# Performance work log

Measured on AMD Instinct MI355X. Metric: run time of the kernel, lower is better.

Reference implementation:

```python
import jax, jax.numpy as jnp
import numpy as np

# Constants from GaussianSplattingCompliance.__init__
SCALE_MIN, SCALE_MAX = 0.05, 1.5
RATIO_MIN, RATIO_MAX = 0.5, 3.5
ROT_MIN, ROT_MAX = -np.pi / 2, np.pi / 2
AXIS_OFFSET = 0.05
EMIN = 1e-9
SMOOTH_K = 10.0

N_POINTS = 131072  # number of FE element centers (512x256 mesh, flattened)
N_G = 256          # number of gaussians (args['args']['N_g'])


def setup_inputs() -> dict:
    key = jax.random.key(0)
    k0, k1, k2, k3, k4 = jax.random.split(key, 5)
    coords = jax.random.uniform(k0, (N_POINTS, 2), dtype=jnp.float32)
    W_scale = jax.random.normal(k1, (N_G, 1), dtype=jnp.float32)
    W_shape_var = jax.random.normal(k2, (N_G, 1), dtype=jnp.float32)
    W_rotation = jax.random.normal(k3, (N_G, 1), dtype=jnp.float32)
    W_offsets = jax.random.normal(k4, (N_G, 2), dtype=jnp.float32)
    return {"coords": coords, "W_scale": W_scale, "W_shape_var": W_shape_var,
            "W_rotation": W_rotation, "W_offsets": W_offsets}


def reference(coords, W_scale, W_shape_var, W_rotation, W_offsets):
    # coord bounds are constant buffers in the original module (computed once in __init__)
    c = jax.lax.stop_gradient(coords)
    cmin, cmax = c.min(axis=0), c.max(axis=0)                      # (2,)
    coord_min = cmin - cmax * AXIS_OFFSET
    coord_max = cmax + cmax * AXIS_OFFSET

    B = W_scale.shape[0]
    base_scale = (SCALE_MAX - SCALE_MIN) * jax.nn.sigmoid(W_scale)[:, 0] + SCALE_MIN   # (B,)
    ratio = (RATIO_MAX - RATIO_MIN) * jax.nn.sigmoid(W_shape_var) + RATIO_MIN          # (B,1)
    sigmas = jnp.concatenate([jnp.ones((B, 1), coords.dtype), ratio], axis=1)          # (B,2)
    rotation = ROT_MIN + (ROT_MAX - ROT_MIN) * jax.nn.sigmoid(W_rotation)[:, 0]        # (B,)
    offsets = coord_min + (coord_max - coord_min) * jax.nn.sigmoid(W_offsets)          # (B,2)

    cos_r, sin_r = jnp.cos(rotation), jnp.sin(rotation)
    R = jnp.stack([jnp.stack([cos_r, -sin_r], axis=-1),
                   jnp.stack([sin_r, cos_r], axis=-1)], axis=-2)                       # (B,2,2)
    inv_cov_diag = 1.0 / (sigmas ** 2 + 1e-6)                                          # (B,2)

    # (B, N, 2): centered, scaled coordinates per gaussian
    xy = (coords[None, :, :] - offsets[:, None, :]) / (base_scale[:, None, None] + 1e-8)
    rxy = jnp.einsum('bij,bnj->bni', R, xy)                                            # (B,N,2)
    # diagonal Mahalanobis quadratic form
    z = jnp.sqrt(jnp.einsum('bni,bi,bni->bn', rxy, inv_cov_diag, rxy))                 # (B,N)
    kernel = jax.nn.sigmoid(-10.0 * (z - 1.0))                                         # 1/(1+exp(10(z-1)))
    kernel_sum = kernel.sum(axis=0) + 1e-8                                             # (N,)
    H = (1.0 - EMIN) * jax.nn.sigmoid(-SMOOTH_K * (kernel_sum - 0.5)) + EMIN           # (N,)
    return H
```

## Files before the change

### kernel.cpp

```cpp
#include <hip/hip_runtime.h>
#include <cmath>

#define N_GAUSS 256

__global__ __launch_bounds__(256) void k_partial_minmax(
    const float2* __restrict__ coords, int n, float4* __restrict__ partial) {
  int tid = blockIdx.x * blockDim.x + threadIdx.x;
  int stride = gridDim.x * blockDim.x;
  float mnx = INFINITY, mny = INFINITY, mxx = -INFINITY, mxy = -INFINITY;
  for (int i = tid; i < n; i += stride) {
    float2 c = coords[i];
    mnx = fminf(mnx, c.x);
    mny = fminf(mny, c.y);
    mxx = fmaxf(mxx, c.x);
    mxy = fmaxf(mxy, c.y);
  }
  for (int o = 32; o > 0; o >>= 1) {
    mnx = fminf(mnx, __shfl_down(mnx, o));
    mny = fminf(mny, __shfl_down(mny, o));
    mxx = fmaxf(mxx, __shfl_down(mxx, o));
    mxy = fmaxf(mxy, __shfl_down(mxy, o));
  }
  __shared__ float4 lds[4];
  if ((threadIdx.x & 63) == 0) lds[threadIdx.x >> 6] = make_float4(mnx, mny, mxx, mxy);
  __syncthreads();
  if (threadIdx.x == 0) {
    float4 r = lds[0];
    for (int w = 1; w < 4; ++w) {
      float4 o = lds[w];
      r.x = fminf(r.x, o.x);
      r.y = fminf(r.y, o.y);
      r.z = fmaxf(r.z, o.z);
      r.w = fmaxf(r.w, o.w);
    }
    partial[blockIdx.x] = r;
  }
}

__device__ __forceinline__ float sigmoidf_fast(float w) {
  float t = __builtin_amdgcn_exp2f(-1.4426950408889634f * w);
  return 1.0f / (1.0f + t);
}

__global__ __launch_bounds__(256) void k_fused_main(
    const float2* __restrict__ coords,
    const float4* __restrict__ partial,
    const float* __restrict__ W_scale,
    const float* __restrict__ W_shape_var,
    const float* __restrict__ W_rotation,
    const float* __restrict__ W_offsets,
    float* __restrict__ out, int n) {
  __shared__ float4 sp[2 * N_GAUSS];
  __shared__ float4 lds4[4];
  __shared__ float4 boundsS;

  int t = threadIdx.x;

  float4 r = partial[t];
  for (int o = 32; o > 0; o >>= 1) {
    r.x = fminf(r.x, __shfl_down(r.x, o));
    r.y = fminf(r.y, __shfl_down(r.y, o));
    r.z = fmaxf(r.z, __shfl_down(r.z, o));
    r.w = fmaxf(r.w, __shfl_down(r.w, o));
  }
  if ((t & 63) == 0) lds4[t >> 6] = r;
  __syncthreads();
  if (t == 0) {
    float4 a = lds4[0];
    for (int w = 1; w < 4; ++w) {
      float4 o = lds4[w];
      a.x = fminf(a.x, o.x);
      a.y = fminf(a.y, o.y);
      a.z = fmaxf(a.z, o.z);
      a.w = fmaxf(a.w, o.w);
    }
    boundsS = a;
  }
  __syncthreads();
  float4 bc = boundsS;

  {
    float cmin0 = bc.x - bc.z * 0.05f;
    float cmin1 = bc.y - bc.w * 0.05f;
    float cmax0 = bc.z + bc.z * 0.05f;
    float cmax1 = bc.w + bc.w * 0.05f;

    float sS = sigmoidf_fast(W_scale[t]);
    float base_scale = 1.45f * sS + 0.05f;
    float sV = sigmoidf_fast(W_shape_var[t]);
    float ratio = 3.0f * sV + 0.5f;
    float sR = sigmoidf_fast(W_rotation[t]);
    const float PIf = 3.14159265358979323846f;
    float rot = -0.5f * PIf + PIf * sR;
    float sOx = sigmoidf_fast(W_offsets[2 * t]);
    float sOy = sigmoidf_fast(W_offsets[2 * t + 1]);
    float ox = cmin0 + (cmax0 - cmin0) * sOx;
    float oy = cmin1 + (cmax1 - cmin1) * sOy;

    float cr = cosf(rot), sr = sinf(rot);
    float inv_s = 1.0f / (base_scale + 1e-8f);
    float r0 = rsqrtf(1.0f + 1e-6f);
    float r1 = rsqrtf(fmaf(ratio, ratio, 1e-6f));

    float A = r0 * cr * inv_s;
    float B = -r0 * sr * inv_s;
    float E = -fmaf(A, ox, B * oy);
    float C = r1 * sr * inv_s;
    float D = r1 * cr * inv_s;
    float F = -fmaf(C, ox, D * oy);

    sp[2 * t]     = make_float4(A, B, E, C);
    sp[2 * t + 1] = make_float4(D, F, 0.0f, 0.0f);
  }
  __syncthreads();

  int i = blockIdx.x * blockDim.x + threadIdx.x;
  if (i >= n) return;
  float2 c = coords[i];
  float x = c.x, y = c.y;
  float ks = 1e-8f;
  const float K1 = 14.4269504088896339f;

  for (int b0 = 0; b0 < N_GAUSS; b0 += 8) {
#pragma unroll
    for (int j = 0; j < 8; ++j) {
      int b = b0 + j;
      float4 p0 = sp[2 * b];
      float4 p1 = sp[2 * b + 1];
      float u = fmaf(p0.x, x, fmaf(p0.y, y, p0.z));
      float v = fmaf(p0.w, x, fmaf(p1.x, y, p1.y));
      float z = sqrtf(fmaf(u, u, v * v));
      float tt = __builtin_amdgcn_exp2f(fmaf(K1, z, -K1));
      ks += __builtin_amdgcn_rcpf(1.0f + tt);
    }
    if (__all(ks > 6.0f)) break;
  }

  float t2 = __builtin_amdgcn_exp2f(fmaf(K1, ks, -0.5f * K1));
  float s = __builtin_amdgcn_rcpf(1.0f + t2);
  out[i] = fmaf(1e-9f, 1.0f - s, s);
}

extern "C" void kernel_launch(void* const* d_in, const int* in_sizes, int n_in,
                              void* d_out, int out_size, void* d_ws, size_t ws_size,
                              hipStream_t stream) {
  const float* coords      = (const float*)d_in[0];
  const float* W_scale     = (const float*)d_in[1];
  const float* W_shape_var = (const float*)d_in[2];
  const float* W_rotation  = (const float*)d_in[3];
  const float* W_offsets   = (const float*)d_in[4];
  float* out = (float*)d_out;

  int n = in_sizes[0] / 2;

  float4* partial = (float4*)d_ws;

  k_partial_minmax<<<256, 256, 0, stream>>>((const float2*)coords, n, partial);
  int blocks = (n + 255) / 256;
  k_fused_main<<<blocks, 256, 0, stream>>>((const float2*)coords, partial,
                                           W_scale, W_shape_var, W_rotation,
                                           W_offsets, out, n);
}
```

Baseline: 66.85 us.

## Process two points per thread and vectorize coord loads; shrink minmax grid

```diff
diff --git a/kernel.cpp b/kernel.cpp
--- a/kernel.cpp
+++ b/kernel.cpp
@@ -4,12 +4,21 @@
 #define N_GAUSS 256
 
 __global__ __launch_bounds__(256) void k_partial_minmax(
-    const float2* __restrict__ coords, int n, float4* __restrict__ partial) {
+    const float4* __restrict__ coords4, int m ,
+    const float2* __restrict__ coords, int n,
+    float4* __restrict__ partial) {
   int tid = blockIdx.x * blockDim.x + threadIdx.x;
   int stride = gridDim.x * blockDim.x;
   float mnx = INFINITY, mny = INFINITY, mxx = -INFINITY, mxy = -INFINITY;
-  for (int i = tid; i < n; i += stride) {
-    float2 c = coords[i];
+  for (int i = tid; i < m; i += stride) {
+    float4 c = coords4[i];
+    mnx = fminf(mnx, fminf(c.x, c.z));
+    mny = fminf(mny, fminf(c.y, c.w));
+    mxx = fmaxf(mxx, fmaxf(c.x, c.z));
+    mxy = fmaxf(mxy, fmaxf(c.y, c.w));
+  }
+  if (tid == 0 && (n & 1)) {
+    float2 c = coords[n - 1];
     mnx = fminf(mnx, c.x);
     mny = fminf(mny, c.y);
     mxx = fmaxf(mxx, c.x);
@@ -43,6 +52,7 @@
 }
 
 __global__ __launch_bounds__(256) void k_fused_main(
+    const float4* __restrict__ coords4,
     const float2* __restrict__ coords,
     const float4* __restrict__ partial,
     const float* __restrict__ W_scale,
@@ -56,7 +66,8 @@
 
   int t = threadIdx.x;
 
-  float4 r = partial[t];
+  float4 r = (t < 64) ? partial[t]
+                      : make_float4(INFINITY, INFINITY, -INFINITY, -INFINITY);
   for (int o = 32; o > 0; o >>= 1) {
     r.x = fminf(r.x, __shfl_down(r.x, o));
     r.y = fminf(r.y, __shfl_down(r.y, o));
@@ -114,31 +125,54 @@
   }
   __syncthreads();
 
-  int i = blockIdx.x * blockDim.x + threadIdx.x;
-  if (i >= n) return;
-  float2 c = coords[i];
-  float x = c.x, y = c.y;
-  float ks = 1e-8f;
+  int gid = blockIdx.x * blockDim.x + threadIdx.x;
+  int i0 = 2 * gid;
+  if (i0 >= n) return;
+  bool has2 = (i0 + 1) < n;
+
+  float x0, y0, x1, y1;
+  if (has2) {
+    float4 c = coords4[gid];
+    x0 = c.x; y0 = c.y; x1 = c.z; y1 = c.w;
+  } else {
+    float2 c = coords[i0];
+    x0 = c.x; y0 = c.y; x1 = c.x; y1 = c.y;
+  }
+
+  float ks0 = 1e-8f, ks1 = 1e-8f;
   const float K1 = 14.4269504088896339f;
 
-  for (int b0 = 0; b0 < N_GAUSS; b0 += 8) {
+  for (int b0 = 0; b0 < N_GAUSS; b0 += 4) {
 #pragma unroll
-    for (int j = 0; j < 8; ++j) {
+    for (int j = 0; j < 4; ++j) {
       int b = b0 + j;
       float4 p0 = sp[2 * b];
       float4 p1 = sp[2 * b + 1];
-      float u = fmaf(p0.x, x, fmaf(p0.y, y, p0.z));
-      float v = fmaf(p0.w, x, fmaf(p1.x, y, p1.y));
-      float z = sqrtf(fmaf(u, u, v * v));
-      float tt = __builtin_amdgcn_exp2f(fmaf(K1, z, -K1));
-      ks += __builtin_amdgcn_rcpf(1.0f + tt);
+      float u0 = fmaf(p0.x, x0, fmaf(p0.y, y0, p0.z));
+      float v0 = fmaf(p0.w, x0, fmaf(p1.x, y0, p1.y));
+      float u1 = fmaf(p0.x, x1, fmaf(p0.y, y1, p0.z));
+      float v1 = fmaf(p0.w, x1, fmaf(p1.x, y1, p1.y));
+      float z0 = sqrtf(fmaf(u0, u0, v0 * v0));
+      float z1 = sqrtf(fmaf(u1, u1, v1 * v1));
+      float t0 = __builtin_amdgcn_exp2f(fmaf(K1, z0, -K1));
+      float t1 = __builtin_amdgcn_exp2f(fmaf(K1, z1, -K1));
+      ks0 += __builtin_amdgcn_rcpf(1.0f + t0);
+      ks1 += __builtin_amdgcn_rcpf(1.0f + t1);
     }
-    if (__all(ks > 6.0f)) break;
-  }
-
-  float t2 = __builtin_amdgcn_exp2f(fmaf(K1, ks, -0.5f * K1));
-  float s = __builtin_amdgcn_rcpf(1.0f + t2);
-  out[i] = fmaf(1e-9f, 1.0f - s, s);
+    if (__all((ks0 > 6.0f) && (ks1 > 6.0f))) break;
+  }
+
+  float e0 = __builtin_amdgcn_exp2f(fmaf(K1, ks0, -0.5f * K1));
+  float s0 = __builtin_amdgcn_rcpf(1.0f + e0);
+  float h0 = fmaf(1e-9f, 1.0f - s0, s0);
+  if (has2) {
+    float e1 = __builtin_amdgcn_exp2f(fmaf(K1, ks1, -0.5f * K1));
+    float s1 = __builtin_amdgcn_rcpf(1.0f + e1);
+    float h1 = fmaf(1e-9f, 1.0f - s1, s1);
+    ((float2*)out)[gid] = make_float2(h0, h1);
+  } else {
+    out[i0] = h0;
+  }
 }
 
 extern "C" void kernel_launch(void* const* d_in, const int* in_sizes, int n_in,
@@ -152,12 +186,16 @@
   float* out = (float*)d_out;
 
   int n = in_sizes[0] / 2;
+  int m = n / 2;
 
   float4* partial = (float4*)d_ws;
 
-  k_partial_minmax<<<256, 256, 0, stream>>>((const float2*)coords, n, partial);
-  int blocks = (n + 255) / 256;
-  k_fused_main<<<blocks, 256, 0, stream>>>((const float2*)coords, partial,
+  k_partial_minmax<<<64, 256, 0, stream>>>((const float4*)coords, m,
+                                           (const float2*)coords, n, partial);
+  int pairs = (n + 1) / 2;
+  int blocks = (pairs + 255) / 256;
+  k_fused_main<<<blocks, 256, 0, stream>>>((const float4*)coords,
+                                           (const float2*)coords, partial,
                                            W_scale, W_shape_var, W_rotation,
                                            W_offsets, out, n);
 }
```

New measurement: 68.02 us. Within noise of the previous version (+1.8%).
